# Optimization experiments

Hardware: AMD Instinct MI355X
Metric: run time of the kernel (lower is better)

## Reference

```python
import jax, jax.numpy as jnp
import numpy as np

# Norse default LIFParameters
TAU_SYN_INV = 200.0  # 1/5e-3
TAU_MEM_INV = 100.0  # 1/1e-2
V_LEAK = 0.0
V_TH = 1.0
V_RESET = 0.0
DT = 0.001


def _heaviside(x):
    return (x > 0).astype(x.dtype)


def setup_inputs() -> dict:
    key = jax.random.key(0)
    k1, k2 = jax.random.split(key)
    T, B, F = 1024, 256, 512
    input_spikes = (jax.random.uniform(k1, (T, B, F)) < 0.1).astype(jnp.float32)
    W = jax.random.normal(k2, (F, F), dtype=jnp.float32) / np.sqrt(F).astype(np.float32)
    return {"input_spikes": input_spikes, "W": W}


def reference(input_spikes, W):
    # input_spikes: [T, B, F]; W: [F, F] (Linear, no bias)
    T, B, F = input_spikes.shape
    # fc batched across the whole sequence (y = x @ W.T)
    xs = jnp.einsum('tbf,gf->tbg', input_spikes, W)  # [T, B, F]
    v0 = jnp.zeros((B, F), dtype=input_spikes.dtype)
    i0 = jnp.zeros((B, F), dtype=input_spikes.dtype)

    def step(carry, x):
        v, i = carry
        v_dec = v + DT * TAU_MEM_INV * ((V_LEAK - v) + i)  # membrane leak+integrate
        i_dec = i - DT * TAU_SYN_INV * i                   # synaptic current decay
        z = _heaviside(v_dec - V_TH)                       # spike
        v_new = (1.0 - z) * v_dec + z * V_RESET            # reset
        i_new = i_dec + x                                  # inject fc output
        return (v_new, i_new), z

    (v, i), zs = jax.lax.scan(step, (v0, i0), xs)
    # matches torch forward: returns (z_last, state) with state = (v, i)
    return zs[-1], v, i
```

## Files before the change

kernel.cpp:

```cpp
#include <hip/hip_runtime.h>
#include <hip/hip_bf16.h>


typedef __attribute__((ext_vector_type(8))) short short8;
typedef __attribute__((ext_vector_type(4))) float floatx4;
typedef __attribute__((ext_vector_type(2))) unsigned uintx2;
typedef __attribute__((ext_vector_type(4))) unsigned uintx4;

#define T_STEPS 1024
#define B_DIM   256
#define F_DIM   512
#define BF      (B_DIM * F_DIM)
#define ROWP    520

static __device__ __forceinline__ unsigned short f2bf_rne(float f) {
    unsigned u = __float_as_uint(f);
    return (unsigned short)((u + 0x7FFFu + ((u >> 16) & 1u)) >> 16);
}
static __device__ __forceinline__ float bf2f(unsigned short h) {
    return __uint_as_float(((unsigned)h) << 16);
}

__global__ __launch_bounds__(256)
void pack_kernel(const float* __restrict__ sp, unsigned* __restrict__ bits)
{
    const int lane = threadIdx.x & 63;
    const int wv   = blockIdx.x * 4 + (threadIdx.x >> 6);
    for (int c = wv; c < 65536; c += 2048 * 4) {
        const float* p = sp + (size_t)c * 2048;
        unsigned val = 0;
        #pragma unroll
        for (int r = 0; r < 32; ++r) {
            float x = p[r * 64 + lane];
            unsigned long long m = __ballot(x != 0.0f);
            unsigned sel = (lane & 1) ? (unsigned)(m >> 32) : (unsigned)m;
            if ((lane >> 1) == r) val = sel;
        }
        bits[(size_t)c * 64 + lane] = val;
    }
}

__global__ __launch_bounds__(512, 2)
void lif_kernel_bits(const unsigned* __restrict__ bits,
                     const float* __restrict__ W,
                     float* __restrict__ out)
{
    __shared__ unsigned short sA[2][16 * ROWP];
    __shared__ float xbuf[2][6 * 256];

    const int tid  = threadIdx.x;
    const int lane = tid & 63;
    const int w    = tid >> 6;
    const int gh   = w & 1;
    const int wq   = w >> 1;
    const int bt   = blockIdx.x & 15;
    const int gb   = blockIdx.x >> 4;
    const int b0   = bt * 16;
    const int gw   = gb * 32 + gh * 16;
    const int mrow = lane & 15;
    const int lq   = lane >> 4;

    short8 whi[4], wmd[4], wlo[4];
    {
        const float* wp = W + (size_t)(gw + mrow) * F_DIM + wq * 128 + lq * 8;
        #pragma unroll
        for (int ks = 0; ks < 4; ++ks) {
            short8 hi, md, lo;
            #pragma unroll
            for (int j = 0; j < 8; ++j) {
                float f = wp[ks * 32 + j];
                unsigned short h = f2bf_rne(f);
                float r1 = f - bf2f(h);
                unsigned short m = f2bf_rne(r1);
                float r2 = r1 - bf2f(m);
                hi[j] = (short)h;
                md[j] = (short)m;
                lo[j] = (short)f2bf_rne(r2);
            }
            whi[ks] = hi; wmd[ks] = md; wlo[ks] = lo;
        }
    }

    float v[4]  = {0.f, 0.f, 0.f, 0.f};
    float cu[4] = {0.f, 0.f, 0.f, 0.f};
    float zf[4] = {0.f, 0.f, 0.f, 0.f};

    const int srow  = tid & 15;
    const int shalf = tid >> 4;
    const int hsh   = (shalf & 1) * 16;
    const unsigned* bp = bits + (size_t)(b0 + srow) * 16 + (shalf >> 1);
    unsigned short* s0 = &sA[0][srow * ROWP + shalf * 16];
    unsigned short* s1 = &sA[1][srow * ROWP + shalf * 16];
    const unsigned short* a0 = &sA[0][mrow * ROWP + wq * 128 + lq * 8];
    const unsigned short* a1 = &sA[1][mrow * ROWP + wq * 128 + lq * 8];
    float* xw0 = &xbuf[0][((wq - 1) * 2 + gh) * 256 + lane * 4];
    float* xw1 = &xbuf[1][((wq - 1) * 2 + gh) * 256 + lane * 4];
    const int xr = gh * 256 + lane * 4;

    auto unpack_to = [&](unsigned dw, unsigned short* dst) {
        unsigned h16 = (dw >> hsh) & 0xFFFFu;
        #pragma unroll
        for (int q = 0; q < 2; ++q) {
            unsigned t8 = (h16 >> (8 * q)) & 0xFFu;
            unsigned u  = t8 | (t8 << 15);
            unsigned x0 =  u        & 0x10001u;
            unsigned x1 = (u >> 2)  & 0x10001u;
            unsigned x2 = (u >> 4)  & 0x10001u;
            unsigned x3 = (u >> 6)  & 0x10001u;
            uintx4 d;
            d[0] = (x0 << 14) - (x0 << 7);
            d[1] = (x1 << 14) - (x1 << 7);
            d[2] = (x2 << 14) - (x2 << 7);
            d[3] = (x3 << 14) - (x3 << 7);
            *(uintx4*)(dst + q * 8) = d;
        }
    };

    auto mfma_acc = [&](const unsigned short* arow,
                        floatx4& ah, floatx4& am, floatx4& al) {
        #pragma unroll
        for (int ks = 0; ks < 4; ++ks) {
            short8 a = *(const short8*)(arow + ks * 32);
            ah = __builtin_amdgcn_mfma_f32_16x16x32_bf16(a, whi[ks], ah, 0, 0, 0);
            am = __builtin_amdgcn_mfma_f32_16x16x32_bf16(a, wmd[ks], am, 0, 0, 0);
            al = __builtin_amdgcn_mfma_f32_16x16x32_bf16(a, wlo[ks], al, 0, 0, 0);
        }
    };

    auto lif_step = [&](const floatx4& ah, const floatx4& am, const floatx4& al,
                        const float* xb) {
        floatx4 p1 = *(const floatx4*)(xb + xr);
        floatx4 p2 = *(const floatx4*)(xb + xr + 512);
        floatx4 p3 = *(const floatx4*)(xb + xr + 1024);
        #pragma unroll
        for (int r = 0; r < 4; ++r) {
            float own  = (ah[r] + am[r]) + al[r];
            float x    = ((own + p1[r]) + p2[r]) + p3[r];
            float vdec = v[r] + 0.1f * ((0.0f - v[r]) + cu[r]);
            float idec = cu[r] - 0.2f * cu[r];
            bool  spk  = (vdec - 1.0f) > 0.0f;
            zf[r] = spk ? 1.0f : 0.0f;
            v[r]  = spk ? 0.0f : vdec;
            cu[r] = idec + x;
        }
    };

    const floatx4 fz = {0.f, 0.f, 0.f, 0.f};
    floatx4 ahA = fz, amA = fz, alA = fz;
    floatx4 ahB = fz, amB = fz, alB = fz;

    unsigned wcur = bp[0];
    unpack_to(wcur, s0);
    wcur = bp[4096];
    unsigned wnxt = bp[2 * 4096];
    __syncthreads();

    for (int t = 0; t < T_STEPS; t += 2) {
        if (wq == 0 && t > 0)
            lif_step(ahB, amB, alB, &xbuf[1][0]);
        ahA = fz; amA = fz; alA = fz;
        unpack_to(wcur, s1);
        wcur = wnxt;
        if (t + 3 < T_STEPS) wnxt = bp[(size_t)(t + 3) * 4096];
        mfma_acc(a0, ahA, amA, alA);
        if (wq > 0)
            *(floatx4*)xw0 = (ahA + amA) + alA;
        __syncthreads();

        if (wq == 0)
            lif_step(ahA, amA, alA, &xbuf[0][0]);
        ahB = fz; amB = fz; alB = fz;
        if (t + 2 < T_STEPS) unpack_to(wcur, s0);
        wcur = wnxt;
        if (t + 4 < T_STEPS) wnxt = bp[(size_t)(t + 4) * 4096];
        mfma_acc(a1, ahB, amB, alB);
        if (wq > 0)
            *(floatx4*)xw1 = (ahB + amB) + alB;
        __syncthreads();
    }
    if (wq == 0) {
        lif_step(ahB, amB, alB, &xbuf[1][0]);
        #pragma unroll
        for (int r = 0; r < 4; ++r) {
            const size_t idx = (size_t)(b0 + lq * 4 + r) * F_DIM + gw + mrow;
            out[idx]          = zf[r];
            out[BF + idx]     = v[r];
            out[2 * BF + idx] = cu[r];
        }
    }
}

__global__ __launch_bounds__(256, 1)
void lif_kernel_f32(const float* __restrict__ spikes,
                    const float* __restrict__ W,
                    float* __restrict__ out)
{
    __shared__ unsigned short sAf[16 * ROWP];
    __shared__ float xbuf[2 * 256];

    const int tid  = threadIdx.x;
    const int lane = tid & 63;
    const int w    = tid >> 6;
    const int gh   = w & 1;
    const int kh   = w >> 1;
    const int bt   = blockIdx.x & 15;
    const int gb   = blockIdx.x >> 4;
    const int b0   = bt * 16;
    const int gw   = gb * 32 + gh * 16;
    const int mrow = lane & 15;
    const int kq   = lane >> 4;

    short8 whi[8], wmd[8], wlo[8];
    {
        const float* wp = W + (size_t)(gw + mrow) * F_DIM + kh * 256 + kq * 8;
        #pragma unroll
        for (int ks = 0; ks < 8; ++ks) {
            short8 hi, md, lo;
            #pragma unroll
            for (int j = 0; j < 8; ++j) {
                float f = wp[ks * 32 + j];
                unsigned short h = f2bf_rne(f);
                float r1 = f - bf2f(h);
                unsigned short m = f2bf_rne(r1);
                float r2 = r1 - bf2f(m);
                hi[j] = (short)h;
                md[j] = (short)m;
                lo[j] = (short)f2bf_rne(r2);
            }
            whi[ks] = hi; wmd[ks] = md; wlo[ks] = lo;
        }
    }

    float v[4]  = {0.f, 0.f, 0.f, 0.f};
    float cu[4] = {0.f, 0.f, 0.f, 0.f};
    float zf[4] = {0.f, 0.f, 0.f, 0.f};

    floatx4 ld[8];
    auto issue_loads = [&](int t) {
        const floatx4* sp = (const floatx4*)(spikes + (size_t)t * BF + (size_t)b0 * F_DIM);
        #pragma unroll
        for (int j = 0; j < 8; ++j)
            ld[j] = sp[tid + 256 * j];
    };

    issue_loads(0);
    for (int t = 0; t < T_STEPS; ++t) {
        #pragma unroll
        for (int j = 0; j < 8; ++j) {
            const int q = tid + 256 * j;
            const int row = q >> 7, col4 = q & 127;
            unsigned u0 = __float_as_uint(ld[j][0]);
            unsigned u1 = __float_as_uint(ld[j][1]);
            unsigned u2 = __float_as_uint(ld[j][2]);
            unsigned u3 = __float_as_uint(ld[j][3]);
            uintx2 d;
            d[0] = (u0 >> 16) | (u1 & 0xFFFF0000u);
            d[1] = (u2 >> 16) | (u3 & 0xFFFF0000u);
            *(uintx2*)&sAf[row * ROWP + col4 * 4] = d;
        }
        __syncthreads();
        if (t + 1 < T_STEPS) issue_loads(t + 1);

        floatx4 ah = {0.f, 0.f, 0.f, 0.f};
        floatx4 am = {0.f, 0.f, 0.f, 0.f};
        floatx4 al = {0.f, 0.f, 0.f, 0.f};
        const unsigned short* arow = &sAf[mrow * ROWP + kh * 256 + kq * 8];
        #pragma unroll
        for (int ks = 0; ks < 8; ++ks) {
            short8 a = *(const short8*)(arow + ks * 32);
            ah = __builtin_amdgcn_mfma_f32_16x16x32_bf16(a, whi[ks], ah, 0, 0, 0);
            am = __builtin_amdgcn_mfma_f32_16x16x32_bf16(a, wmd[ks], am, 0, 0, 0);
            al = __builtin_amdgcn_mfma_f32_16x16x32_bf16(a, wlo[ks], al, 0, 0, 0);
        }

        if (kh == 1) {
            floatx4 xp = (ah + am) + al;
            *(floatx4*)&xbuf[gh * 256 + lane * 4] = xp;
        }
        __syncthreads();
        if (kh == 0) {
            floatx4 other = *(const floatx4*)&xbuf[gh * 256 + lane * 4];
            #pragma unroll
            for (int r = 0; r < 4; ++r) {
                float x    = ((ah[r] + am[r]) + al[r]) + other[r];
                float vdec = v[r] + 0.1f * ((0.0f - v[r]) + cu[r]);
                float idec = cu[r] - 0.2f * cu[r];
                bool  spk  = (vdec - 1.0f) > 0.0f;
                zf[r] = spk ? 1.0f : 0.0f;
                v[r]  = spk ? 0.0f : vdec;
                cu[r] = idec + x;
            }
        }
    }

    if (kh == 0) {
        #pragma unroll
        for (int r = 0; r < 4; ++r) {
            const size_t idx = (size_t)(b0 + kq * 4 + r) * F_DIM + gw + mrow;
            out[idx]          = zf[r];
            out[BF + idx]     = v[r];
            out[2 * BF + idx] = cu[r];
        }
    }
}

extern "C" void kernel_launch(void* const* d_in, const int* in_sizes, int n_in,
                              void* d_out, int out_size, void* d_ws, size_t ws_size,
                              hipStream_t stream)
{
    const float* spikes = (const float*)d_in[0];
    const float* W      = (const float*)d_in[1];
    float* out          = (float*)d_out;

    const size_t need = (size_t)T_STEPS * B_DIM * (F_DIM / 8);
    if (d_ws != nullptr && ws_size >= need) {
        unsigned* bits = (unsigned*)d_ws;
        pack_kernel<<<dim3(2048), dim3(256), 0, stream>>>(spikes, bits);
        lif_kernel_bits<<<dim3(256), dim3(512), 0, stream>>>(bits, W, out);
    } else {
        lif_kernel_f32<<<dim3(256), dim3(256), 0, stream>>>(spikes, W, out);
    }
}
```

Baseline: 1.214 ms.

## Split LIF work across twice the blocks and expand spike bits directly into MFMA registers

Each block now owns 16 output neurons instead of 32, so the launch uses 512 blocks, and each of 8 waves covers a 64-wide K slice instead of a 128-wide one. Every lane loads its own packed bit words and expands them into bf16 A-fragments in registers, which removes the shared-memory A staging buffer and its unpack stores. The intent is more parallelism and a shorter per-step critical path in the serial time loop. In exchange, the partial-sum reduction in wave 0 grows from three to seven shared-memory reads per step, and each block has fewer waves doing useful MFMA work relative to its barrier cost.

```diff
diff --git a/kernel.cpp b/kernel.cpp
--- a/kernel.cpp
+++ b/kernel.cpp
@@ -40,31 +40,29 @@
     }
 }
 
-__global__ __launch_bounds__(512, 2)
+__global__ __launch_bounds__(512, 4)
 void lif_kernel_bits(const unsigned* __restrict__ bits,
                      const float* __restrict__ W,
                      float* __restrict__ out)
 {
-    __shared__ unsigned short sA[2][16 * ROWP];
-    __shared__ float xbuf[2][6 * 256];
+    __shared__ float xbuf[2][7 * 256];
 
     const int tid  = threadIdx.x;
     const int lane = tid & 63;
-    const int w    = tid >> 6;
-    const int gh   = w & 1;
-    const int wq   = w >> 1;
+    const int wq   = tid >> 6;
     const int bt   = blockIdx.x & 15;
     const int gb   = blockIdx.x >> 4;
     const int b0   = bt * 16;
-    const int gw   = gb * 32 + gh * 16;
+    const int gw   = gb * 16;
     const int mrow = lane & 15;
     const int lq   = lane >> 4;
-
-    short8 whi[4], wmd[4], wlo[4];
+    const int bsh  = lq * 8;
+
+    short8 whi[2], wmd[2], wlo[2];
     {
-        const float* wp = W + (size_t)(gw + mrow) * F_DIM + wq * 128 + lq * 8;
-        #pragma unroll
-        for (int ks = 0; ks < 4; ++ks) {
+        const float* wp = W + (size_t)(gw + mrow) * F_DIM + wq * 64 + lq * 8;
+        #pragma unroll
+        for (int ks = 0; ks < 2; ++ks) {
             short8 hi, md, lo;
             #pragma unroll
             for (int j = 0; j < 8; ++j) {
@@ -85,24 +83,17 @@
     float cu[4] = {0.f, 0.f, 0.f, 0.f};
     float zf[4] = {0.f, 0.f, 0.f, 0.f};
 
-    const int srow  = tid & 15;
-    const int shalf = tid >> 4;
-    const int hsh   = (shalf & 1) * 16;
-    const unsigned* bp = bits + (size_t)(b0 + srow) * 16 + (shalf >> 1);
-    unsigned short* s0 = &sA[0][srow * ROWP + shalf * 16];
-    unsigned short* s1 = &sA[1][srow * ROWP + shalf * 16];
-    const unsigned short* a0 = &sA[0][mrow * ROWP + wq * 128 + lq * 8];
-    const unsigned short* a1 = &sA[1][mrow * ROWP + wq * 128 + lq * 8];
-    float* xw0 = &xbuf[0][((wq - 1) * 2 + gh) * 256 + lane * 4];
-    float* xw1 = &xbuf[1][((wq - 1) * 2 + gh) * 256 + lane * 4];
-    const int xr = gh * 256 + lane * 4;
-
-    auto unpack_to = [&](unsigned dw, unsigned short* dst) {
-        unsigned h16 = (dw >> hsh) & 0xFFFFu;
-        #pragma unroll
-        for (int q = 0; q < 2; ++q) {
-            unsigned t8 = (h16 >> (8 * q)) & 0xFFu;
-            unsigned u  = t8 | (t8 << 15);
+    const unsigned* bp = bits + (size_t)(b0 + mrow) * 16 + wq * 2;
+
+    auto ldbits = [&](int t) -> uintx2 {
+        return *(const uintx2*)(bp + (size_t)t * 4096);
+    };
+
+    auto expand = [&](uintx2 bq, short8* af) {
+        #pragma unroll
+        for (int ks = 0; ks < 2; ++ks) {
+            unsigned b8 = (bq[ks] >> bsh) & 0xFFu;
+            unsigned u  = b8 | (b8 << 15);
             unsigned x0 =  u        & 0x10001u;
             unsigned x1 = (u >> 2)  & 0x10001u;
             unsigned x2 = (u >> 4)  & 0x10001u;
@@ -112,30 +103,35 @@
             d[1] = (x1 << 14) - (x1 << 7);
             d[2] = (x2 << 14) - (x2 << 7);
             d[3] = (x3 << 14) - (x3 << 7);
-            *(uintx4*)(dst + q * 8) = d;
-        }
-    };
-
-    auto mfma_acc = [&](const unsigned short* arow,
-                        floatx4& ah, floatx4& am, floatx4& al) {
-        #pragma unroll
-        for (int ks = 0; ks < 4; ++ks) {
-            short8 a = *(const short8*)(arow + ks * 32);
-            ah = __builtin_amdgcn_mfma_f32_16x16x32_bf16(a, whi[ks], ah, 0, 0, 0);
-            am = __builtin_amdgcn_mfma_f32_16x16x32_bf16(a, wmd[ks], am, 0, 0, 0);
-            al = __builtin_amdgcn_mfma_f32_16x16x32_bf16(a, wlo[ks], al, 0, 0, 0);
-        }
+            af[ks] = *(short8*)&d;
+        }
+    };
+
+    const floatx4 fz = {0.f, 0.f, 0.f, 0.f};
+
+    auto mfma3 = [&](const short8* af, floatx4& ah, floatx4& am, floatx4& al) {
+        ah = __builtin_amdgcn_mfma_f32_16x16x32_bf16(af[0], whi[0], fz, 0, 0, 0);
+        am = __builtin_amdgcn_mfma_f32_16x16x32_bf16(af[0], wmd[0], fz, 0, 0, 0);
+        al = __builtin_amdgcn_mfma_f32_16x16x32_bf16(af[0], wlo[0], fz, 0, 0, 0);
+        ah = __builtin_amdgcn_mfma_f32_16x16x32_bf16(af[1], whi[1], ah, 0, 0, 0);
+        am = __builtin_amdgcn_mfma_f32_16x16x32_bf16(af[1], wmd[1], am, 0, 0, 0);
+        al = __builtin_amdgcn_mfma_f32_16x16x32_bf16(af[1], wlo[1], al, 0, 0, 0);
     };
 
     auto lif_step = [&](const floatx4& ah, const floatx4& am, const floatx4& al,
                         const float* xb) {
-        floatx4 p1 = *(const floatx4*)(xb + xr);
-        floatx4 p2 = *(const floatx4*)(xb + xr + 512);
-        floatx4 p3 = *(const floatx4*)(xb + xr + 1024);
+        floatx4 s;
+        #pragma unroll
+        for (int r = 0; r < 4; ++r) s[r] = (ah[r] + am[r]) + al[r];
+        #pragma unroll
+        for (int j = 0; j < 7; ++j) {
+            floatx4 p = *(const floatx4*)(xb + j * 256 + lane * 4);
+            #pragma unroll
+            for (int r = 0; r < 4; ++r) s[r] += p[r];
+        }
         #pragma unroll
         for (int r = 0; r < 4; ++r) {
-            float own  = (ah[r] + am[r]) + al[r];
-            float x    = ((own + p1[r]) + p2[r]) + p3[r];
+            float x    = s[r];
             float vdec = v[r] + 0.1f * ((0.0f - v[r]) + cu[r]);
             float idec = cu[r] - 0.2f * cu[r];
             bool  spk  = (vdec - 1.0f) > 0.0f;
@@ -145,37 +141,38 @@
         }
     };
 
-    const floatx4 fz = {0.f, 0.f, 0.f, 0.f};
     floatx4 ahA = fz, amA = fz, alA = fz;
     floatx4 ahB = fz, amB = fz, alB = fz;
-
-    unsigned wcur = bp[0];
-    unpack_to(wcur, s0);
-    wcur = bp[4096];
-    unsigned wnxt = bp[2 * 4096];
-    __syncthreads();
+    short8 afA[2], afB[2];
+
+    uintx2 bqA = ldbits(0);
+    uintx2 bqB = ldbits(1);
 
     for (int t = 0; t < T_STEPS; t += 2) {
         if (wq == 0 && t > 0)
             lif_step(ahB, amB, alB, &xbuf[1][0]);
-        ahA = fz; amA = fz; alA = fz;
-        unpack_to(wcur, s1);
-        wcur = wnxt;
-        if (t + 3 < T_STEPS) wnxt = bp[(size_t)(t + 3) * 4096];
-        mfma_acc(a0, ahA, amA, alA);
-        if (wq > 0)
-            *(floatx4*)xw0 = (ahA + amA) + alA;
+        expand(bqA, afA);
+        if (t + 2 < T_STEPS) bqA = ldbits(t + 2);
+        mfma3(afA, ahA, amA, alA);
+        if (wq > 0) {
+            floatx4 xp;
+            #pragma unroll
+            for (int r = 0; r < 4; ++r) xp[r] = (ahA[r] + amA[r]) + alA[r];
+            *(floatx4*)&xbuf[0][(wq - 1) * 256 + lane * 4] = xp;
+        }
         __syncthreads();
 
         if (wq == 0)
             lif_step(ahA, amA, alA, &xbuf[0][0]);
-        ahB = fz; amB = fz; alB = fz;
-        if (t + 2 < T_STEPS) unpack_to(wcur, s0);
-        wcur = wnxt;
-        if (t + 4 < T_STEPS) wnxt = bp[(size_t)(t + 4) * 4096];
-        mfma_acc(a1, ahB, amB, alB);
-        if (wq > 0)
-            *(floatx4*)xw1 = (ahB + amB) + alB;
+        expand(bqB, afB);
+        if (t + 3 < T_STEPS) bqB = ldbits(t + 3);
+        mfma3(afB, ahB, amB, alB);
+        if (wq > 0) {
+            floatx4 xp;
+            #pragma unroll
+            for (int r = 0; r < 4; ++r) xp[r] = (ahB[r] + amB[r]) + alB[r];
+            *(floatx4*)&xbuf[1][(wq - 1) * 256 + lane * 4] = xp;
+        }
         __syncthreads();
     }
     if (wq == 0) {
@@ -316,7 +313,7 @@
     if (d_ws != nullptr && ws_size >= need) {
         unsigned* bits = (unsigned*)d_ws;
         pack_kernel<<<dim3(2048), dim3(256), 0, stream>>>(spikes, bits);
-        lif_kernel_bits<<<dim3(256), dim3(512), 0, stream>>>(bits, W, out);
+        lif_kernel_bits<<<dim3(512), dim3(512), 0, stream>>>(bits, W, out);
     } else {
         lif_kernel_f32<<<dim3(256), dim3(256), 0, stream>>>(spikes, W, out);
     }
```

Measured after the change: 1.223 ms. Within noise of the previous version (+0.7%).
